# Kernel tuning notes

Hardware: AMD Instinct MI355X
Metric: run time of the kernel (lower is better)

## Reference

```python
import jax, jax.numpy as jnp
import numpy as np

N, F, T, H = 1024, 22, 1000, 64
EPS = 1e-5


def setup_inputs() -> dict:
    key = jax.random.key(0)
    ks = iter(jax.random.split(key, 64))
    def rn(shape, s=0.1):
        return jax.random.normal(next(ks), shape, jnp.float32) * s
    inp = {"x": rn((N, F, T), 1.0)}
    in_dims = [F, H, H]
    for l in range(3):
        inp[f"Wih{l}"] = rn((4 * H, in_dims[l]))
        inp[f"Whh{l}"] = rn((4 * H, H))
        inp[f"bih{l}"] = rn((4 * H,))
        inp[f"bhh{l}"] = rn((4 * H,))
    fc = [(64, 54), (54, 44), (44, 24), (24, 4)]
    for i, (di, do) in enumerate(fc):
        inp[f"w{i}"] = rn((do, di))
        inp[f"b{i}"] = rn((do,))
    for i, d in enumerate([54, 44, 24]):
        inp[f"g{i}"] = jnp.ones((d,), jnp.float32)
        inp[f"be{i}"] = jnp.zeros((d,), jnp.float32)
        inp[f"m{i}"] = rn((d,))
        inp[f"v{i}"] = jax.random.uniform(next(ks), (d,), jnp.float32) + 0.5
    return inp


def _lstm_layer(xs, Wih, Whh, b):
    # xs: (T, N, in) -> hs: (T, N, H)
    n = xs.shape[1]
    h0 = jnp.zeros((n, Whh.shape[1]), xs.dtype)
    def step(carry, xt):
        h, c = carry
        z = xt @ Wih.T + h @ Whh.T + b  # (N, 4H)
        i, f, g, o = jnp.split(z, 4, axis=-1)  # PyTorch gate order i,f,g,o
        c = jax.nn.sigmoid(f) * c + jax.nn.sigmoid(i) * jnp.tanh(g)
        h = jax.nn.sigmoid(o) * jnp.tanh(c)
        return (h, c), h
    (_, _), hs = jax.lax.scan(step, (h0, h0), xs)
    return hs


def _bn(x, g, be, m, v):
    return (x - m) * jax.lax.rsqrt(v + EPS) * g + be


def reference(x, Wih0, Whh0, bih0, bhh0, Wih1, Whh1, bih1, bhh1,
              Wih2, Whh2, bih2, bhh2,
              w0, b0, g0, be0, m0, v0,
              w1, b1, g1, be1, m1, v1,
              w2, b2, g2, be2, m2, v2,
              w3, b3):
    # (N, F, T) -> permute(0,2,1) -> (N, T, F); scan over time-major (T, N, F)
    xs = jnp.transpose(x, (2, 0, 1))
    xs = _lstm_layer(xs, Wih0, Whh0, bih0 + bhh0)
    xs = _lstm_layer(xs, Wih1, Whh1, bih1 + bhh1)
    xs = _lstm_layer(xs, Wih2, Whh2, bih2 + bhh2)
    h = xs[-1]  # last timestep, (N, H)
    h = jax.nn.relu(_bn(h @ w0.T + b0, g0, be0, m0, v0))
    h = jax.nn.relu(_bn(h @ w1.T + b1, g1, be1, m1, v1))
    h = jax.nn.relu(_bn(h @ w2.T + b2, g2, be2, m2, v2))
    return h @ w3.T + b3
```

## Files before the change

kernel.cpp:

```cpp
#include <hip/hip_runtime.h>
#include <hip/hip_fp16.h>

#define TT 1000
#define FF 22
#define HH 64
#define BB 4
#define NBLK 256
#define S0 112
#define S1 144
#define SL0 (4 * S0)
#define SL1 (4 * S1)

typedef _Float16 half8 __attribute__((ext_vector_type(8)));
typedef float float4v __attribute__((ext_vector_type(4)));

__device__ __forceinline__ float sigm(float v) {
    return __builtin_amdgcn_rcpf(1.0f + __expf(-v));
}
__device__ __forceinline__ float tanh_(float v) {
    return 1.0f - 2.0f * __builtin_amdgcn_rcpf(__expf(2.0f * v) + 1.0f);
}

__device__ __forceinline__ float sel4(const float4v a, int q) {
    float lo = (q & 2) ? a[2] : a[0];
    float hi = (q & 2) ? a[3] : a[1];
    return (q & 1) ? hi : lo;
}

__device__ __forceinline__ float gate_update(const float z[4], float& c) {
    float cc = sigm(z[1]) * c + sigm(z[0]) * tanh_(z[2]);
    c = cc;
    return sigm(z[3]) * tanh_(cc);
}

__device__ __forceinline__ int ldmin4(const int* p) {
    int4 v = *(const int4*)p;
    return min(min(v.x, v.y), min(v.z, v.w));
}

#define SPIN(cond) do { for (;;) { asm volatile("" ::: "memory"); if (cond) break; \
                        __builtin_amdgcn_s_sleep(1); } asm volatile("" ::: "memory"); } while (0)

extern "C" __global__ void __launch_bounds__(896, 1)
lstm_fused(const float* __restrict__ x,
           const float* __restrict__ Wih0, const float* __restrict__ Whh0,
           const float* __restrict__ bih0, const float* __restrict__ bhh0,
           const float* __restrict__ Wih1, const float* __restrict__ Whh1,
           const float* __restrict__ bih1, const float* __restrict__ bhh1,
           const float* __restrict__ Wih2, const float* __restrict__ Whh2,
           const float* __restrict__ bih2, const float* __restrict__ bhh2,
           const float* __restrict__ w0, const float* __restrict__ b0,
           const float* __restrict__ w1, const float* __restrict__ b1,
           const float* __restrict__ w2, const float* __restrict__ b2,
           const float* __restrict__ w3, const float* __restrict__ b3,
           const float* __restrict__ g0, const float* __restrict__ be0,
           const float* __restrict__ m0, const float* __restrict__ v0,
           const float* __restrict__ g1, const float* __restrict__ be1,
           const float* __restrict__ m1, const float* __restrict__ v1,
           const float* __restrict__ g2, const float* __restrict__ be2,
           const float* __restrict__ m2, const float* __restrict__ v2,
           float* __restrict__ out)
{
    __shared__ __align__(16) _Float16 in0[8 * SL0];
    __shared__ __align__(16) _Float16 in1[8 * SL1];
    __shared__ __align__(16) _Float16 in2[8 * SL1];
    __shared__ __align__(16) int flags[16];
    __shared__ float fcA[BB * 64];
    __shared__ float fcB[BB * 64];
    __shared__ float fcW[54 * 65];
    __shared__ float fcP[5 * 64];

    const int tid  = threadIdx.x;
    const int wv   = tid >> 6;
    const int role = wv >> 2;
    const int w4   = wv & 3;
    const int l    = tid & 63;
    const int q    = l >> 4;
    const int l15  = l & 15;
    const int u    = 16 * w4 + l15;
    const int b    = q;
    const int n0   = blockIdx.x * BB;

    for (int i = tid; i < 8 * SL0; i += 896) in0[i] = (_Float16)0.0f;
    for (int i = tid; i < 8 * SL1; i += 896) in1[i] = (_Float16)0.0f;
    for (int i = tid; i < 8 * SL1; i += 896) in2[i] = (_Float16)0.0f;
    if (tid < 16) flags[tid] = (tid >= 14) ? (1 << 29) : -1;

    half8 wf[4][4];
    float4v biasC[4];
    if (role == 2) {
#pragma unroll
        for (int g = 0; g < 4; ++g) {
            const int row = 64 * g + u;
#pragma unroll
            for (int kt = 0; kt < 3; ++kt) {
                half8 h{};
#pragma unroll
                for (int j = 0; j < 8; ++j) {
                    const int k = 32 * kt + 8 * q + j;
                    float val = 0.0f;
                    if (k < 32) { if (k < FF) val = Wih0[row * FF + k]; }
                    else        { val = Whh0[row * HH + (k - 32)]; }
                    h[j] = (_Float16)val;
                }
                wf[g][kt] = h;
            }
            float bv = bih0[row] + bhh0[row];
            biasC[g] = float4v{bv, bv, bv, bv};
        }
    } else if (role < 2) {
        const float* Wih = role ? Wih1 : Wih2;
        const float* Whh = role ? Whh1 : Whh2;
        const float* bih = role ? bih1 : bih2;
        const float* bhh = role ? bhh1 : bhh2;
#pragma unroll
        for (int g = 0; g < 4; ++g) {
            const int row = 64 * g + u;
#pragma unroll
            for (int kt = 0; kt < 4; ++kt) {
                half8 h{};
#pragma unroll
                for (int j = 0; j < 8; ++j) {
                    const int k = 32 * kt + 8 * q + j;
                    h[j] = (_Float16)((k < 64) ? Wih[row * HH + k] : Whh[row * HH + (k - 64)]);
                }
                wf[g][kt] = h;
            }
            float bv = bih[row] + bhh[row];
            biasC[g] = float4v{bv, bv, bv, bv};
        }
    }

    const int  st  = tid - 768;
    const bool xok = (role == 3) && (st >= 0) && (st < BB * FF);
    const int  xb  = xok ? (st / FF) : 0;
    const int  xf  = xok ? (st - xb * FF) : 0;
    const float* xp = x + ((size_t)(n0 + xb) * FF + xf) * TT;

    volatile int* vfl = (volatile int*)flags;
    __syncthreads();

    const int arow = (role == 2) ? ((l15 & 3) * S0 + q * 8) : ((l15 & 3) * S1 + q * 8);
    float c = 0.f;

    if (role == 3) {
        float xh = xok ? xp[0] : 0.f;
        for (int k = 0; k < 125; ++k) {
            const int tb = k * 8;
#pragma unroll
            for (int s = 0; s < 8; ++s) {
                const int t = tb + s;
                if ((s & 3) == 0) SPIN(ldmin4(flags + 8) >= t - 5);
                if (xok) in0[s * SL0 + xb * S0 + xf] = (_Float16)xh;
                __threadfence_block();
                if (l == 0) vfl[12 + (wv - 12)] = t;
                if (xok) xh = xp[(t + 1 < TT) ? (t + 1) : (TT - 1)];
            }
        }
    } else if (role == 2) {
        for (int k = 0; k < 125; ++k) {
            const int tb = k * 8;
#pragma unroll
            for (int s = 0; s < 8; ++s) {
                const int t = tb + s;
                if ((s & 3) == 0)
                    SPIN(ldmin4(flags + 12) >= t + 3 && ldmin4(flags + 4) >= t - 5);
                SPIN(ldmin4(flags + 8) >= t - 1);
                const _Float16* rd = in0 + s * SL0;
                half8 a0 = *(const half8*)(rd + arow);
                half8 a1 = *(const half8*)(rd + arow + 32);
                half8 a2 = *(const half8*)(rd + arow + 64);
                float4v acc[4];
#pragma unroll
                for (int g = 0; g < 4; ++g)
                    acc[g] = __builtin_amdgcn_mfma_f32_16x16x32_f16(a0, wf[g][0], biasC[g], 0, 0, 0);
#pragma unroll
                for (int g = 0; g < 4; ++g)
                    acc[g] = __builtin_amdgcn_mfma_f32_16x16x32_f16(a1, wf[g][1], acc[g], 0, 0, 0);
#pragma unroll
                for (int g = 0; g < 4; ++g)
                    acc[g] = __builtin_amdgcn_mfma_f32_16x16x32_f16(a2, wf[g][2], acc[g], 0, 0, 0);
                float z[4];
#pragma unroll
                for (int g = 0; g < 4; ++g) z[g] = sel4(acc[g], q);
                float h = gate_update(z, c);
                _Float16 hf = (_Float16)h;
                in0[((s + 1) & 7) * SL0 + b * S0 + 32 + u] = hf;
                in1[s * SL1 + b * S1 + u]                  = hf;
                __threadfence_block();
                if (l == 0) vfl[8 + w4] = t;
            }
        }
    } else {
        _Float16* rin  = role ? in1 : in2;
        _Float16* rout = role ? in2 : nullptr;
        const int* pin = role ? (flags + 8) : (flags + 4);
        const int* pow_ = role ? (flags + 4) : (flags + 0);
        for (int k = 0; k < 125; ++k) {
            const int tb = k * 8;
#pragma unroll
            for (int s = 0; s < 8; ++s) {
                const int t = tb + s;
                if ((s & 3) == 0) {
                    if (role) SPIN(ldmin4(pin) >= t + 3 && ldmin4(flags + 0) >= t - 5);
                    else      SPIN(ldmin4(pin) >= t + 3);
                }
                SPIN(ldmin4(pow_) >= t - 1);
                const _Float16* rd = rin + s * SL1;
                half8 a0 = *(const half8*)(rd + arow);
                half8 a1 = *(const half8*)(rd + arow + 32);
                half8 a2 = *(const half8*)(rd + arow + 64);
                half8 a3 = *(const half8*)(rd + arow + 96);
                float4v acc[4];
#pragma unroll
                for (int g = 0; g < 4; ++g)
                    acc[g] = __builtin_amdgcn_mfma_f32_16x16x32_f16(a0, wf[g][0], biasC[g], 0, 0, 0);
#pragma unroll
                for (int g = 0; g < 4; ++g)
                    acc[g] = __builtin_amdgcn_mfma_f32_16x16x32_f16(a1, wf[g][1], acc[g], 0, 0, 0);
#pragma unroll
                for (int g = 0; g < 4; ++g)
                    acc[g] = __builtin_amdgcn_mfma_f32_16x16x32_f16(a2, wf[g][2], acc[g], 0, 0, 0);
#pragma unroll
                for (int g = 0; g < 4; ++g)
                    acc[g] = __builtin_amdgcn_mfma_f32_16x16x32_f16(a3, wf[g][3], acc[g], 0, 0, 0);
                float z[4];
#pragma unroll
                for (int g = 0; g < 4; ++g) z[g] = sel4(acc[g], q);
                float h = gate_update(z, c);
                _Float16 hf = (_Float16)h;
                if (role) {
                    rin[((s + 1) & 7) * SL1 + b * S1 + 64 + u] = hf;
                    rout[s * SL1 + b * S1 + u]                 = hf;
                } else {
                    if (t != TT - 1) rin[((s + 1) & 7) * SL1 + b * S1 + 64 + u] = hf;
                    else             fcA[b * 64 + u] = h;
                }
                __threadfence_block();
                if (l == 0) vfl[(role ? 4 : 0) + w4] = t;
            }
        }
    }

    __syncthreads();

    for (int i = tid; i < 54 * 64; i += 896) fcW[(i >> 6) * 65 + (i & 63)] = w0[i];
    for (int i = tid; i < 54; i += 896) {
        fcP[i] = b0[i]; fcP[64 + i] = g0[i]; fcP[128 + i] = be0[i];
        fcP[192 + i] = m0[i]; fcP[256 + i] = v0[i];
    }
    __syncthreads();
    for (int idx = tid; idx < BB * 54; idx += 896) {
        const int bb = idx / 54, j = idx - bb * 54;
        float s = fcP[j];
        for (int k = 0; k < 64; ++k) s += fcW[j * 65 + k] * fcA[bb * 64 + k];
        s = (s - fcP[192 + j]) * rsqrtf(fcP[256 + j] + 1e-5f) * fcP[64 + j] + fcP[128 + j];
        fcB[bb * 64 + j] = fmaxf(s, 0.0f);
    }
    __syncthreads();

    for (int i = tid; i < 44 * 54; i += 896) fcW[(i / 54) * 55 + (i % 54)] = w1[i];
    for (int i = tid; i < 44; i += 896) {
        fcP[i] = b1[i]; fcP[64 + i] = g1[i]; fcP[128 + i] = be1[i];
        fcP[192 + i] = m1[i]; fcP[256 + i] = v1[i];
    }
    __syncthreads();
    for (int idx = tid; idx < BB * 44; idx += 896) {
        const int bb = idx / 44, j = idx - bb * 44;
        float s = fcP[j];
        for (int k = 0; k < 54; ++k) s += fcW[j * 55 + k] * fcB[bb * 64 + k];
        s = (s - fcP[192 + j]) * rsqrtf(fcP[256 + j] + 1e-5f) * fcP[64 + j] + fcP[128 + j];
        fcA[bb * 64 + j] = fmaxf(s, 0.0f);
    }
    __syncthreads();

    for (int i = tid; i < 24 * 44; i += 896) fcW[(i / 44) * 45 + (i % 44)] = w2[i];
    for (int i = tid; i < 24; i += 896) {
        fcP[i] = b2[i]; fcP[64 + i] = g2[i]; fcP[128 + i] = be2[i];
        fcP[192 + i] = m2[i]; fcP[256 + i] = v2[i];
    }
    __syncthreads();
    for (int idx = tid; idx < BB * 24; idx += 896) {
        const int bb = idx / 24, j = idx - bb * 24;
        float s = fcP[j];
        for (int k = 0; k < 44; ++k) s += fcW[j * 45 + k] * fcA[bb * 64 + k];
        s = (s - fcP[192 + j]) * rsqrtf(fcP[256 + j] + 1e-5f) * fcP[64 + j] + fcP[128 + j];
        fcB[bb * 64 + j] = fmaxf(s, 0.0f);
    }
    __syncthreads();

    for (int i = tid; i < 4 * 24; i += 896) fcW[(i / 24) * 25 + (i % 24)] = w3[i];
    for (int i = tid; i < 4; i += 896) fcP[i] = b3[i];
    __syncthreads();
    for (int idx = tid; idx < BB * 4; idx += 896) {
        const int bb = idx / 4, j = idx - bb * 4;
        float s = fcP[j];
        for (int k = 0; k < 24; ++k) s += fcW[j * 25 + k] * fcB[bb * 64 + k];
        out[(size_t)(n0 + bb) * 4 + j] = s;
    }
}

extern "C" void kernel_launch(void* const* d_in, const int* in_sizes, int n_in,
                              void* d_out, int out_size, void* d_ws, size_t ws_size,
                              hipStream_t stream) {
    const float* p[33];
    for (int i = 0; i < 33; ++i) p[i] = (const float*)d_in[i];
    lstm_fused<<<NBLK, 896, 0, stream>>>(
        p[0],
        p[1], p[2], p[3], p[4],
        p[5], p[6], p[7], p[8],
        p[9], p[10], p[11], p[12],
        p[13], p[14], p[15], p[16], p[17], p[18], p[19], p[20],
        p[21], p[22], p[23], p[24],
        p[25], p[26], p[27], p[28],
        p[29], p[30], p[31], p[32],
        (float*)d_out);
}
```

Before: 817.1 us.

## Drop x-loader warps; layer-0 waves prefetch x into registers and overlap MFMAs with spins

Removes the dedicated x-staging role (wave group 3) and its flag handshake. Layer-0 waves now load their x slice straight from global into registers two steps ahead and issue the input-projection MFMA before waiting on the recurrent flag. Layers 1 and 2 likewise issue the input-half MFMAs before spinning on their own recurrent dependency. The block shrinks from 896 to 768 threads, and __threadfence_block is replaced by an LDS-only waitcnt. This shortens the per-timestep critical path, at the cost of strided global loads of x that now sit inside the layer-0 recurrence loop.

```diff
diff --git a/kernel.cpp b/kernel.cpp
--- a/kernel.cpp
+++ b/kernel.cpp
@@ -40,8 +40,9 @@
 
 #define SPIN(cond) do { for (;;) { asm volatile("" ::: "memory"); if (cond) break; \
                         __builtin_amdgcn_s_sleep(1); } asm volatile("" ::: "memory"); } while (0)
-
-extern "C" __global__ void __launch_bounds__(896, 1)
+#define DSFENCE() asm volatile("s_waitcnt lgkmcnt(0)" ::: "memory")
+
+extern "C" __global__ void __launch_bounds__(768, 1)
 lstm_fused(const float* __restrict__ x,
            const float* __restrict__ Wih0, const float* __restrict__ Whh0,
            const float* __restrict__ bih0, const float* __restrict__ bhh0,
@@ -81,10 +82,10 @@
     const int b    = q;
     const int n0   = blockIdx.x * BB;
 
-    for (int i = tid; i < 8 * SL0; i += 896) in0[i] = (_Float16)0.0f;
-    for (int i = tid; i < 8 * SL1; i += 896) in1[i] = (_Float16)0.0f;
-    for (int i = tid; i < 8 * SL1; i += 896) in2[i] = (_Float16)0.0f;
-    if (tid < 16) flags[tid] = (tid >= 14) ? (1 << 29) : -1;
+    for (int i = tid; i < 8 * SL0; i += 768) in0[i] = (_Float16)0.0f;
+    for (int i = tid; i < 8 * SL1; i += 768) in1[i] = (_Float16)0.0f;
+    for (int i = tid; i < 8 * SL1; i += 768) in2[i] = (_Float16)0.0f;
+    if (tid < 16) flags[tid] = (tid >= 12) ? (1 << 29) : -1;
 
     half8 wf[4][4];
     float4v biasC[4];
@@ -108,7 +109,7 @@
             float bv = bih0[row] + bhh0[row];
             biasC[g] = float4v{bv, bv, bv, bv};
         }
-    } else if (role < 2) {
+    } else {
         const float* Wih = role ? Wih1 : Wih2;
         const float* Whh = role ? Whh1 : Whh2;
         const float* bih = role ? bih1 : bih2;
@@ -131,49 +132,41 @@
         }
     }
 
-    const int  st  = tid - 768;
-    const bool xok = (role == 3) && (st >= 0) && (st < BB * FF);
-    const int  xb  = xok ? (st / FF) : 0;
-    const int  xf  = xok ? (st - xb * FF) : 0;
-    const float* xp = x + ((size_t)(n0 + xb) * FF + xf) * TT;
-
     volatile int* vfl = (volatile int*)flags;
     __syncthreads();
 
     const int arow = (role == 2) ? ((l15 & 3) * S0 + q * 8) : ((l15 & 3) * S1 + q * 8);
     float c = 0.f;
 
-    if (role == 3) {
-        float xh = xok ? xp[0] : 0.f;
+    if (role == 2) {
+        const int rrow = l15 & 3;
+        const float* xbase = x + (size_t)(n0 + rrow) * FF * TT;
+        float xA[8], xB[8];
+#define LDX(tt, buf) do { _Pragma("unroll") \
+        for (int j = 0; j < 8; ++j) { \
+            const int f = 8 * q + j; \
+            (buf)[j] = (f < FF) ? xbase[(size_t)f * TT + (tt)] : 0.0f; \
+        } } while (0)
+        LDX(0, xA);
+        LDX(1, xB);
         for (int k = 0; k < 125; ++k) {
             const int tb = k * 8;
 #pragma unroll
             for (int s = 0; s < 8; ++s) {
                 const int t = tb + s;
-                if ((s & 3) == 0) SPIN(ldmin4(flags + 8) >= t - 5);
-                if (xok) in0[s * SL0 + xb * S0 + xf] = (_Float16)xh;
-                __threadfence_block();
-                if (l == 0) vfl[12 + (wv - 12)] = t;
-                if (xok) xh = xp[(t + 1 < TT) ? (t + 1) : (TT - 1)];
-            }
-        }
-    } else if (role == 2) {
-        for (int k = 0; k < 125; ++k) {
-            const int tb = k * 8;
-#pragma unroll
-            for (int s = 0; s < 8; ++s) {
-                const int t = tb + s;
-                if ((s & 3) == 0)
-                    SPIN(ldmin4(flags + 12) >= t + 3 && ldmin4(flags + 4) >= t - 5);
+                float* xb = (s & 1) ? xB : xA;
+                half8 a0;
+#pragma unroll
+                for (int j = 0; j < 8; ++j) a0[j] = (_Float16)xb[j];
+                float4v acc[4];
+#pragma unroll
+                for (int g = 0; g < 4; ++g)
+                    acc[g] = __builtin_amdgcn_mfma_f32_16x16x32_f16(a0, wf[g][0], biasC[g], 0, 0, 0);
+                if ((s & 3) == 0) SPIN(ldmin4(flags + 4) >= t - 5);
                 SPIN(ldmin4(flags + 8) >= t - 1);
                 const _Float16* rd = in0 + s * SL0;
-                half8 a0 = *(const half8*)(rd + arow);
                 half8 a1 = *(const half8*)(rd + arow + 32);
                 half8 a2 = *(const half8*)(rd + arow + 64);
-                float4v acc[4];
-#pragma unroll
-                for (int g = 0; g < 4; ++g)
-                    acc[g] = __builtin_amdgcn_mfma_f32_16x16x32_f16(a0, wf[g][0], biasC[g], 0, 0, 0);
 #pragma unroll
                 for (int g = 0; g < 4; ++g)
                     acc[g] = __builtin_amdgcn_mfma_f32_16x16x32_f16(a1, wf[g][1], acc[g], 0, 0, 0);
@@ -187,10 +180,12 @@
                 _Float16 hf = (_Float16)h;
                 in0[((s + 1) & 7) * SL0 + b * S0 + 32 + u] = hf;
                 in1[s * SL1 + b * S1 + u]                  = hf;
-                __threadfence_block();
+                DSFENCE();
                 if (l == 0) vfl[8 + w4] = t;
+                LDX((t + 2 < TT) ? (t + 2) : (TT - 1), xb);
             }
         }
+#undef LDX
     } else {
         _Float16* rin  = role ? in1 : in2;
         _Float16* rout = role ? in2 : nullptr;
@@ -205,19 +200,19 @@
                     if (role) SPIN(ldmin4(pin) >= t + 3 && ldmin4(flags + 0) >= t - 5);
                     else      SPIN(ldmin4(pin) >= t + 3);
                 }
-                SPIN(ldmin4(pow_) >= t - 1);
                 const _Float16* rd = rin + s * SL1;
                 half8 a0 = *(const half8*)(rd + arow);
                 half8 a1 = *(const half8*)(rd + arow + 32);
+                float4v acc[4];
+#pragma unroll
+                for (int g = 0; g < 4; ++g)
+                    acc[g] = __builtin_amdgcn_mfma_f32_16x16x32_f16(a0, wf[g][0], biasC[g], 0, 0, 0);
+#pragma unroll
+                for (int g = 0; g < 4; ++g)
+                    acc[g] = __builtin_amdgcn_mfma_f32_16x16x32_f16(a1, wf[g][1], acc[g], 0, 0, 0);
+                SPIN(ldmin4(pow_) >= t - 1);
                 half8 a2 = *(const half8*)(rd + arow + 64);
                 half8 a3 = *(const half8*)(rd + arow + 96);
-                float4v acc[4];
-#pragma unroll
-                for (int g = 0; g < 4; ++g)
-                    acc[g] = __builtin_amdgcn_mfma_f32_16x16x32_f16(a0, wf[g][0], biasC[g], 0, 0, 0);
-#pragma unroll
-                for (int g = 0; g < 4; ++g)
-                    acc[g] = __builtin_amdgcn_mfma_f32_16x16x32_f16(a1, wf[g][1], acc[g], 0, 0, 0);
 #pragma unroll
                 for (int g = 0; g < 4; ++g)
                     acc[g] = __builtin_amdgcn_mfma_f32_16x16x32_f16(a2, wf[g][2], acc[g], 0, 0, 0);
@@ -236,7 +231,7 @@
                     if (t != TT - 1) rin[((s + 1) & 7) * SL1 + b * S1 + 64 + u] = hf;
                     else             fcA[b * 64 + u] = h;
                 }
-                __threadfence_block();
+                DSFENCE();
                 if (l == 0) vfl[(role ? 4 : 0) + w4] = t;
             }
         }
@@ -244,13 +239,13 @@
 
     __syncthreads();
 
-    for (int i = tid; i < 54 * 64; i += 896) fcW[(i >> 6) * 65 + (i & 63)] = w0[i];
-    for (int i = tid; i < 54; i += 896) {
+    for (int i = tid; i < 54 * 64; i += 768) fcW[(i >> 6) * 65 + (i & 63)] = w0[i];
+    for (int i = tid; i < 54; i += 768) {
         fcP[i] = b0[i]; fcP[64 + i] = g0[i]; fcP[128 + i] = be0[i];
         fcP[192 + i] = m0[i]; fcP[256 + i] = v0[i];
     }
     __syncthreads();
-    for (int idx = tid; idx < BB * 54; idx += 896) {
+    for (int idx = tid; idx < BB * 54; idx += 768) {
         const int bb = idx / 54, j = idx - bb * 54;
         float s = fcP[j];
         for (int k = 0; k < 64; ++k) s += fcW[j * 65 + k] * fcA[bb * 64 + k];
@@ -259,13 +254,13 @@
     }
     __syncthreads();
 
-    for (int i = tid; i < 44 * 54; i += 896) fcW[(i / 54) * 55 + (i % 54)] = w1[i];
-    for (int i = tid; i < 44; i += 896) {
+    for (int i = tid; i < 44 * 54; i += 768) fcW[(i / 54) * 55 + (i % 54)] = w1[i];
+    for (int i = tid; i < 44; i += 768) {
         fcP[i] = b1[i]; fcP[64 + i] = g1[i]; fcP[128 + i] = be1[i];
         fcP[192 + i] = m1[i]; fcP[256 + i] = v1[i];
     }
     __syncthreads();
-    for (int idx = tid; idx < BB * 44; idx += 896) {
+    for (int idx = tid; idx < BB * 44; idx += 768) {
         const int bb = idx / 44, j = idx - bb * 44;
         float s = fcP[j];
         for (int k = 0; k < 54; ++k) s += fcW[j * 55 + k] * fcB[bb * 64 + k];
@@ -274,13 +269,13 @@
     }
     __syncthreads();
 
-    for (int i = tid; i < 24 * 44; i += 896) fcW[(i / 44) * 45 + (i % 44)] = w2[i];
-    for (int i = tid; i < 24; i += 896) {
+    for (int i = tid; i < 24 * 44; i += 768) fcW[(i / 44) * 45 + (i % 44)] = w2[i];
+    for (int i = tid; i < 24; i += 768) {
         fcP[i] = b2[i]; fcP[64 + i] = g2[i]; fcP[128 + i] = be2[i];
         fcP[192 + i] = m2[i]; fcP[256 + i] = v2[i];
     }
     __syncthreads();
-    for (int idx = tid; idx < BB * 24; idx += 896) {
+    for (int idx = tid; idx < BB * 24; idx += 768) {
         const int bb = idx / 24, j = idx - bb * 24;
         float s = fcP[j];
         for (int k = 0; k < 44; ++k) s += fcW[j * 45 + k] * fcA[bb * 64 + k];
@@ -289,10 +284,10 @@
     }
     __syncthreads();
 
-    for (int i = tid; i < 4 * 24; i += 896) fcW[(i / 24) * 25 + (i % 24)] = w3[i];
-    for (int i = tid; i < 4; i += 896) fcP[i] = b3[i];
-    __syncthreads();
-    for (int idx = tid; idx < BB * 4; idx += 896) {
+    for (int i = tid; i < 4 * 24; i += 768) fcW[(i / 24) * 25 + (i % 24)] = w3[i];
+    for (int i = tid; i < 4; i += 768) fcP[i] = b3[i];
+    __syncthreads();
+    for (int idx = tid; idx < BB * 4; idx += 768) {
         const int bb = idx / 4, j = idx - bb * 4;
         float s = fcP[j];
         for (int k = 0; k < 24; ++k) s += fcW[j * 25 + k] * fcB[bb * 64 + k];
@@ -305,7 +300,7 @@
                               hipStream_t stream) {
     const float* p[33];
     for (int i = 0; i < 33; ++i) p[i] = (const float*)d_in[i];
-    lstm_fused<<<NBLK, 896, 0, stream>>>(
+    lstm_fused<<<NBLK, 768, 0, stream>>>(
         p[0],
         p[1], p[2], p[3], p[4],
         p[5], p[6], p[7], p[8],
```

Result: slower. 1.198 ms (+46.6%).
